# Performance work log

Hardware: AMD Instinct MI355X
Metric: run time of the kernel (lower is better)

## Reference

```python
import jax, jax.numpy as jnp
import numpy as np

SCALE = 1.0 / np.sqrt(1024.0).astype(np.float32)


def setup_inputs() -> dict:
    key = jax.random.key(0)
    k1, k2, k3, k4, k5, k6 = jax.random.split(key, 6)
    B, Lq, Lk, D_in, D = 8, 2048, 2048, 1024, 256
    data1 = jax.random.normal(k1, (B, Lq, D_in), dtype=jnp.float32)
    data2 = jax.random.normal(k2, (B, Lk, D), dtype=jnp.float32)
    Wq = jax.random.normal(k3, (D_in, D), dtype=jnp.float32) * (1.0 / np.sqrt(D_in))
    bq = jax.random.normal(k4, (D,), dtype=jnp.float32) * 0.01
    Wk = jax.random.normal(k5, (D, D), dtype=jnp.float32) * (1.0 / np.sqrt(D))
    bk = jax.random.normal(k6, (D,), dtype=jnp.float32) * 0.01
    return {"data1": data1, "data2": data2, "Wq": Wq, "bq": bq, "Wk": Wk, "bk": bk}


def reference(data1, data2, Wq, bq, Wk, bk):
    # query: [B, Lq, D], key: [B, Lk, D]
    query = jnp.einsum('bli,id->bld', data1, Wq) + bq
    key = jnp.einsum('bli,id->bld', data2, Wk) + bk
    # scores: [B, Lq, Lk], scaled by sqrt(1024) as in the original
    scores = jnp.einsum('bqd,bkd->bqk', query, key) * SCALE
    attn = jax.nn.softmax(scores, axis=-1)
    # key reused as value; fused residual add with query
    context = jnp.einsum('bqk,bkd->bqd', attn, key) + query
    return context
```

## Files before the change

kernel.cpp:

```cpp
#include <hip/hip_runtime.h>
#include <hip/hip_bf16.h>

typedef __bf16 bf16x8 __attribute__((ext_vector_type(8)));
typedef __bf16 bf16x2 __attribute__((ext_vector_type(2)));
typedef unsigned short u16x8 __attribute__((ext_vector_type(8)));
typedef float f32x4 __attribute__((ext_vector_type(4)));
typedef float f32x16 __attribute__((ext_vector_type(16)));

#define MFMA(a, b, c) __builtin_amdgcn_mfma_f32_16x16x32_bf16(a, b, c, 0, 0, 0)
#define MFMA32(a, b, c) __builtin_amdgcn_mfma_f32_32x32x16_bf16(a, b, c, 0, 0, 0)

#define LQ 2048
#define DD 256

static __device__ __forceinline__ float bf2f(unsigned short u) {
  union { unsigned int i; float f; } x; x.i = ((unsigned int)u) << 16; return x.f;
}
static __device__ __forceinline__ unsigned short f2bf(float f) {
  union { float f; unsigned int i; } x; x.f = f;
  unsigned int r = x.i + 0x7fffu + ((x.i >> 16) & 1u);
  return (unsigned short)(r >> 16);
}
static __device__ __forceinline__ void gll16(const void* g, void* l) {
  __builtin_amdgcn_global_load_lds(
      (const __attribute__((address_space(1))) unsigned int*)g,
      (__attribute__((address_space(3))) unsigned int*)l, 16, 0, 0);
}
static __device__ __forceinline__ unsigned pack2(float a, float b) {
  union { bf16x2 v; unsigned u; } x;
  x.v[0] = (__bf16)a; x.v[1] = (__bf16)b;
  return x.u;
}

__global__ void wt2_kernel(const float* __restrict__ Wq, unsigned short* __restrict__ WqT,
                           const float* __restrict__ Wk, unsigned short* __restrict__ WkT) {
  int id = blockIdx.x * 256 + threadIdx.x;
  if (id < 262144) {
    int n = id >> 10, k = id & 1023;
    WqT[id] = f2bf(Wq[k * 256 + n]);
  } else {
    int j = id - 262144;
    int n = j >> 8, k = j & 255;
    WkT[j] = f2bf(Wk[k * 256 + n]);
  }
}

static __device__ __forceinline__ void proj_body(
    const float* __restrict__ A, const unsigned short* __restrict__ WT,
    const float* __restrict__ bias, unsigned short* __restrict__ outb,
    unsigned short* __restrict__ outT, int Kd, int bid,
    unsigned short* A_s , unsigned short* B_s ) {
  const int tid = threadIdx.x;
  const int w = tid >> 6, lane = tid & 63, g = lane >> 4, c = lane & 15;
  const int m0 = (bid >> 1) * 64, n0 = (bid & 1) * 128;
  const int wr = (w >> 1) * 32, wc = (w & 1) * 64;

  f32x4 acc[2][4];
  const f32x4 z4 = {0.f, 0.f, 0.f, 0.f};
#pragma unroll
  for (int i = 0; i < 2; i++)
#pragma unroll
    for (int j = 0; j < 4; j++) acc[i][j] = z4;

  const int row_a = tid >> 2, k0a = (tid & 3) * 8;
  const unsigned swz_a = (unsigned)((row_a & 7) << 4);
  const float* asrc = A + (long)(m0 + row_a) * Kd + k0a;
  const int brow0 = w * 32 + (lane >> 2);

#define GLLB(buf, ks_)                                                         \
  _Pragma("unroll") for (int j = 0; j < 2; j++) {                              \
    const int brow = brow0 + j * 16;                                           \
    gll16((const char*)WT + (long)(n0 + brow) * (long)(Kd * 2) + (ks_) * 64 +  \
              (((lane & 3) * 16) ^ ((brow & 3) << 4)),                         \
          (char*)B_s + (buf) * 8192 + w * 2048 + j * 1024);                    \
  }

#define WRA(buf, plo, phi)                                                     \
  {                                                                            \
    bf16x8 t;                                                                  \
    _Pragma("unroll") for (int jj = 0; jj < 4; jj++) {                         \
      t[jj] = (__bf16)(plo)[jj]; t[4 + jj] = (__bf16)(phi)[jj];                \
    }                                                                          \
    *(bf16x8*)((char*)A_s + (buf) * 4096 +                                     \
               (((unsigned)(row_a * 64 + k0a * 2)) ^ swz_a)) = t;              \
  }

#define COMPUTE(buf)                                                           \
  {                                                                            \
    bf16x8 af[2], bfr[4];                                                      \
    _Pragma("unroll") for (int rf = 0; rf < 2; rf++) {                         \
      const int row = wr + rf * 16 + c;                                        \
      af[rf] = *(const bf16x8*)((char*)A_s + (buf) * 4096 +                    \
               (((unsigned)(row * 64 + g * 16)) ^ ((row & 7) << 4)));          \
    }                                                                          \
    _Pragma("unroll") for (int cf = 0; cf < 4; cf++) {                         \
      const int row = wc + cf * 16 + c;                                        \
      bfr[cf] = *(const bf16x8*)((char*)B_s + (buf) * 8192 + row * 64 +        \
               (((unsigned)(g * 16)) ^ ((unsigned)((row & 3) << 4))));         \
    }                                                                          \
    _Pragma("unroll") for (int rf = 0; rf < 2; rf++)                           \
      _Pragma("unroll") for (int cf = 0; cf < 4; cf++)                         \
        acc[rf][cf] = MFMA(af[rf], bfr[cf], acc[rf][cf]);                      \
  }

  const int nk = Kd >> 5;
  f32x4 pe0, pe1, po0, po1;
  pe0 = *(const f32x4*)(asrc);       pe1 = *(const f32x4*)(asrc + 4);
  GLLB(0, 0);
  po0 = *(const f32x4*)(asrc + 32);  po1 = *(const f32x4*)(asrc + 36);
  WRA(0, pe0, pe1);
  pe0 = *(const f32x4*)(asrc + 64);  pe1 = *(const f32x4*)(asrc + 68);
  __syncthreads();

  for (int t = 0; t < nk; t += 2) {
    GLLB(1, t + 1);
    WRA(1, po0, po1);
    if (t + 3 < nk) {
      po0 = *(const f32x4*)(asrc + (t + 3) * 32);
      po1 = *(const f32x4*)(asrc + (t + 3) * 32 + 4);
    }
    COMPUTE(0);
    __syncthreads();
    if (t + 2 < nk) {
      GLLB(0, t + 2);
      WRA(0, pe0, pe1);
      if (t + 4 < nk) {
        pe0 = *(const f32x4*)(asrc + (t + 4) * 32);
        pe1 = *(const f32x4*)(asrc + (t + 4) * 32 + 4);
      }
    }
    COMPUTE(1);
    __syncthreads();
  }
#undef GLLB
#undef WRA
#undef COMPUTE

#pragma unroll
  for (int cf = 0; cf < 4; cf++) {
    const int col = n0 + wc + cf * 16 + c;
    const float bv = bias[col];
#pragma unroll
    for (int rf = 0; rf < 2; rf++) {
      const int row0 = m0 + wr + rf * 16 + g * 4;
      unsigned short pk[4];
#pragma unroll
      for (int i = 0; i < 4; i++) {
        float v = acc[rf][cf][i] + bv;
        pk[i] = f2bf(v);
        outb[(long)(row0 + i) * 256 + col] = pk[i];
      }
      if (outT) {
        const int b = row0 >> 11;
        const int key0 = row0 & 2047;
        unsigned long long packed = (unsigned long long)pk[0] |
                                    ((unsigned long long)pk[1] << 16) |
                                    ((unsigned long long)pk[2] << 32) |
                                    ((unsigned long long)pk[3] << 48);
        *(unsigned long long*)(outT + ((long)(b * 256 + col) * LQ + key0)) = packed;
      }
    }
  }
}

__global__ __launch_bounds__(256) void proj2_kernel(
    const float* __restrict__ data1, const unsigned short* __restrict__ WqT,
    const float* __restrict__ bq, unsigned short* __restrict__ Qb,
    const float* __restrict__ data2, const unsigned short* __restrict__ WkT,
    const float* __restrict__ bk, unsigned short* __restrict__ Kb,
    unsigned short* __restrict__ KTb) {
  __shared__ unsigned short A_s[2 * 64 * 32];
  __shared__ unsigned short B_s[2 * 128 * 32];
  const int bid = blockIdx.x;
  if (bid < 512) {
    proj_body(data1, WqT, bq, Qb, (unsigned short*)nullptr, 1024, bid, A_s, B_s);
  } else {
    proj_body(data2, WkT, bk, Kb, KTb, 256, bid - 512, A_s, B_s);
  }
}

template <int NSPLIT, bool ALLBF>
__global__ __launch_bounds__(256, 2) void attn_kernel(
    const unsigned short* __restrict__ Qb, const unsigned short* __restrict__ Kb,
    const unsigned short* __restrict__ KTb, unsigned short* __restrict__ Op,
    float* __restrict__ out, float* __restrict__ ML) {
  constexpr int KS = 2048 / NSPLIT;
  constexpr int NT = KS / 32;
  constexpr int NBLK = 128 * NSPLIT;
  __shared__ char Ks[2][16384];
  __shared__ char KTs[2][16384];
  const int tid = threadIdx.x;
  const int w = tid >> 6, lane = tid & 63;
  const int l5 = lane >> 5, q31 = lane & 31;
  const int lid = (blockIdx.x & 7) * (NBLK / 8) + (blockIdx.x >> 3);
  const int ksplit = lid & (NSPLIT - 1), qg = lid / NSPLIT;
  const int b = qg >> 4;
  const long qrow0 = (long)qg * 128;
  const int kbase = ksplit * KS;
  const float CS = 0.03125f * 1.4426950408889634f;
  const float THRM = 8.0f / CS;

  bf16x8 qf[16];
  {
    const unsigned short* qp = Qb + (qrow0 + w * 32 + q31) * DD + l5 * 8;
#pragma unroll
    for (int s = 0; s < 16; s++) qf[s] = *(const bf16x8*)(qp + s * 16);
  }
  f32x16 o[8];
#pragma unroll
  for (int t = 0; t < 8; t++) o[t] = (f32x16)(0.f);
  float m_ = -1e30f, l_ = 0.f;

  const char* kb_b = (const char*)(Kb + (long)b * LQ * DD);
  const char* kt_b = (const char*)(KTb + (long)b * DD * LQ);

#define STAGE(buf, kt_)                                                          \
  {                                                                              \
    const int k0_ = kbase + (kt_) * 32;                                          \
    const char* kbp_ = kb_b + (long)(k0_ + q31) * 512 + l5 * 16;                 \
    _Pragma("unroll") for (int i = 0; i < 4; i++) {                              \
      const int sl = w * 4 + i;                                                  \
      gll16(kbp_ + sl * 32, Ks[buf] + sl * 1024);                                \
    }                                                                            \
    _Pragma("unroll") for (int i = 0; i < 4; i++) {                              \
      const int th = w * 4 + i;                                                  \
      gll16(kt_b + (long)((th >> 1) * 32 + q31) * 4096 + (long)k0_ * 2 +         \
                (th & 1) * 32 + l5 * 16,                                         \
            KTs[buf] + th * 1024);                                               \
    }                                                                            \
  }

  STAGE(0, 0);
  for (int kt = 0; kt < NT; kt++) {
    const int cur = kt & 1;
    __syncthreads();
    if (kt + 1 < NT) STAGE(cur ^ 1, kt + 1);

    const char* kr = Ks[cur] + lane * 16;
    f32x16 s = (f32x16)(0.f);
#pragma unroll
    for (int sl = 0; sl < 16; sl++) {
      bf16x8 kf = *(const bf16x8*)(kr + sl * 1024);
      s = MFMA32(kf, qf[sl], s);
    }

    float mx = s[0];
#pragma unroll
    for (int r = 1; r < 16; r++) mx = fmaxf(mx, s[r]);
    mx = fmaxf(mx, __shfl_xor(mx, 32));
    if (__any(mx > m_ + THRM)) {
      float mn = fmaxf(m_, mx);
      float al = exp2f((m_ - mn) * CS);
      m_ = mn;
      l_ *= al;
#pragma unroll
      for (int t = 0; t < 8; t++) o[t] *= al;
    }
    const float mCS = m_ * CS;
    float p[16];
    float ls = 0.f;
#pragma unroll
    for (int r = 0; r < 16; r++) {
      p[r] = exp2f(s[r] * CS - mCS);
      ls += p[r];
    }
    l_ += ls;

    unsigned pk[8];
#pragma unroll
    for (int j = 0; j < 8; j++) pk[j] = pack2(p[2 * j], p[2 * j + 1]);
    unsigned x0 = (unsigned)__shfl_xor((int)pk[0], 32);
    unsigned x1 = (unsigned)__shfl_xor((int)pk[1], 32);
    unsigned x2 = (unsigned)__shfl_xor((int)pk[2], 32);
    unsigned x3 = (unsigned)__shfl_xor((int)pk[3], 32);
    unsigned x4 = (unsigned)__shfl_xor((int)pk[4], 32);
    unsigned x5 = (unsigned)__shfl_xor((int)pk[5], 32);
    unsigned x6 = (unsigned)__shfl_xor((int)pk[6], 32);
    unsigned x7 = (unsigned)__shfl_xor((int)pk[7], 32);
    union { unsigned u[4]; bf16x8 v; } pf0, pf1;
    const bool hi = (l5 != 0);
    pf0.u[0] = hi ? x2 : pk[0];
    pf0.u[1] = hi ? x3 : pk[1];
    pf0.u[2] = hi ? pk[2] : x0;
    pf0.u[3] = hi ? pk[3] : x1;
    pf1.u[0] = hi ? x6 : pk[4];
    pf1.u[1] = hi ? x7 : pk[5];
    pf1.u[2] = hi ? pk[6] : x4;
    pf1.u[3] = hi ? pk[7] : x5;

    const char* vr = KTs[cur] + lane * 16;
#pragma unroll
    for (int t = 0; t < 8; t++) {
      bf16x8 v0 = *(const bf16x8*)(vr + (t * 2) * 1024);
      bf16x8 v1 = *(const bf16x8*)(vr + (t * 2 + 1) * 1024);
      o[t] = MFMA32(v0, pf0.v, o[t]);
      o[t] = MFMA32(v1, pf1.v, o[t]);
    }
  }
#undef STAGE

  l_ += __shfl_xor(l_, 32);

  const long orow = (qrow0 + w * 32 + q31) * (long)DD;
  if (!ALLBF && ksplit == NSPLIT - 1) {
    float* op = out + orow;
#pragma unroll
    for (int t = 0; t < 8; t++)
#pragma unroll
      for (int r = 0; r < 16; r++)
        op[t * 32 + (r & 3) + 8 * (r >> 2) + 4 * l5] = o[t][r];
  } else {
    unsigned short* opb = Op + (long)ksplit * (16384 * 256) + orow;
#pragma unroll
    for (int t = 0; t < 8; t++)
#pragma unroll
      for (int r = 0; r < 16; r++)
        opb[t * 32 + (r & 3) + 8 * (r >> 2) + 4 * l5] = f2bf(o[t][r]);
  }
  if (lane < 32) {
    float* mlp = ML + (long)(qg * NSPLIT + ksplit) * 256;
    mlp[w * 32 + q31] = m_;
    mlp[128 + w * 32 + q31] = l_;
  }
}

template <int NSPLIT, bool ALLBF>
__global__ __launch_bounds__(256) void merge_kernel(
    const unsigned short* __restrict__ Op, const float* __restrict__ ML,
    const unsigned short* __restrict__ Qb, float* __restrict__ out) {
  const float CS = 0.03125f * 1.4426950408889634f;
  const long gid = (long)blockIdx.x * 256 + threadIdx.x;
  const long idx = gid * 8;
  const int row = (int)(idx >> 8);
  const int qg = row >> 7, qr = row & 127;
  const float* mlb = ML + (long)(qg * NSPLIT) * 256;
  float mv[NSPLIT], lv[NSPLIT];
#pragma unroll
  for (int k = 0; k < NSPLIT; k++) {
    mv[k] = mlb[k * 256 + qr];
    lv[k] = mlb[k * 256 + 128 + qr];
  }
  float M = mv[0];
#pragma unroll
  for (int k = 1; k < NSPLIT; k++) M = fmaxf(M, mv[k]);
  float ek[NSPLIT], wsum = 0.f;
#pragma unroll
  for (int k = 0; k < NSPLIT; k++) {
    ek[k] = exp2f((mv[k] - M) * CS);
    wsum += ek[k] * lv[k];
  }
  const float inv = 1.0f / wsum;
  float acc[8];
  if (ALLBF) {
#pragma unroll
    for (int e = 0; e < 8; e++) acc[e] = 0.f;
#pragma unroll
    for (int k = 0; k < NSPLIT; k++) {
      u16x8 p = *(const u16x8*)(Op + (long)k * (16384 * 256) + idx);
#pragma unroll
      for (int e = 0; e < 8; e++) acc[e] += ek[k] * bf2f(p[e]);
    }
  } else {
    f32x4 pa = *(const f32x4*)(out + idx);
    f32x4 pb = *(const f32x4*)(out + idx + 4);
#pragma unroll
    for (int e = 0; e < 4; e++) {
      acc[e] = ek[NSPLIT - 1] * pa[e];
      acc[4 + e] = ek[NSPLIT - 1] * pb[e];
    }
#pragma unroll
    for (int k = 0; k < NSPLIT - 1; k++) {
      u16x8 p = *(const u16x8*)(Op + (long)k * (16384 * 256) + idx);
#pragma unroll
      for (int e = 0; e < 8; e++) acc[e] += ek[k] * bf2f(p[e]);
    }
  }
  u16x8 qv = *(const u16x8*)(Qb + idx);
  f32x4 ra, rb;
#pragma unroll
  for (int e = 0; e < 4; e++) ra[e] = acc[e] * inv + bf2f(qv[e]);
#pragma unroll
  for (int e = 0; e < 4; e++) rb[e] = acc[4 + e] * inv + bf2f(qv[4 + e]);
  *(f32x4*)(out + idx) = ra;
  *(f32x4*)(out + idx + 4) = rb;
}

extern "C" void kernel_launch(void* const* d_in, const int* in_sizes, int n_in,
                              void* d_out, int out_size, void* d_ws, size_t ws_size,
                              hipStream_t stream) {
  (void)in_sizes; (void)n_in; (void)out_size;
  const float* data1 = (const float*)d_in[0];
  const float* data2 = (const float*)d_in[1];
  const float* Wq = (const float*)d_in[2];
  const float* bq = (const float*)d_in[3];
  const float* Wk = (const float*)d_in[4];
  const float* bk = (const float*)d_in[5];
  float* out = (float*)d_out;

  char* ws = (char*)d_ws;
  unsigned short* Qb  = (unsigned short*)(ws);
  unsigned short* Kb  = (unsigned short*)(ws + (8ull << 20));
  unsigned short* KTb = (unsigned short*)(ws + (16ull << 20));
  unsigned short* WqT = (unsigned short*)(ws + (24ull << 20));
  unsigned short* WkT = (unsigned short*)(ws + (24ull << 20) + (512u << 10));
  unsigned short* Op  = (unsigned short*)(ws + (25ull << 20));

  wt2_kernel<<<dim3(1280), dim3(256), 0, stream>>>(Wq, WqT, Wk, WkT);
  proj2_kernel<<<dim3(1024), dim3(256), 0, stream>>>(data1, WqT, bq, Qb,
                                                     data2, WkT, bk, Kb, KTb);

  if (ws_size >= (58ull << 20)) {
    float* MLb = (float*)(ws + (57ull << 20));
    attn_kernel<4, true><<<dim3(512), dim3(256), 0, stream>>>(Qb, Kb, KTb, Op, out, MLb);
    merge_kernel<4, true><<<dim3(2048), dim3(256), 0, stream>>>(Op, MLb, Qb, out);
  } else if (ws_size >= (50ull << 20)) {
    float* MLb = (float*)(ws + (49ull << 20));
    attn_kernel<4, false><<<dim3(512), dim3(256), 0, stream>>>(Qb, Kb, KTb, Op, out, MLb);
    merge_kernel<4, false><<<dim3(2048), dim3(256), 0, stream>>>(Op, MLb, Qb, out);
  } else {
    float* MLb = (float*)(ws + (33ull << 20));
    attn_kernel<2, false><<<dim3(256), dim3(256), 0, stream>>>(Qb, Kb, KTb, Op, out, MLb);
    merge_kernel<2, false><<<dim3(2048), dim3(256), 0, stream>>>(Op, MLb, Qb, out);
  }
}
```

Before: 103.3 us.

## Fuse split-K merge into attention kernel via last-arriving-block atomic counter

```diff
diff --git a/kernel.cpp b/kernel.cpp
--- a/kernel.cpp
+++ b/kernel.cpp
@@ -12,6 +12,7 @@
 
 #define LQ 2048
 #define DD 256
+#define OPSTRIDE (16384L * 256L)
 
 static __device__ __forceinline__ float bf2f(unsigned short u) {
   union { unsigned int i; float f; } x; x.i = ((unsigned int)u) << 16; return x.f;
@@ -179,16 +180,18 @@
   }
 }
 
-template <int NSPLIT, bool ALLBF>
+template <int NSPLIT, bool ALLBF, bool FUSEMERGE>
 __global__ __launch_bounds__(256, 2) void attn_kernel(
     const unsigned short* __restrict__ Qb, const unsigned short* __restrict__ Kb,
     const unsigned short* __restrict__ KTb, unsigned short* __restrict__ Op,
-    float* __restrict__ out, float* __restrict__ ML) {
+    float* __restrict__ out, float* __restrict__ ML,
+    unsigned int* __restrict__ cnt) {
   constexpr int KS = 2048 / NSPLIT;
   constexpr int NT = KS / 32;
   constexpr int NBLK = 128 * NSPLIT;
   __shared__ char Ks[2][16384];
   __shared__ char KTs[2][16384];
+  __shared__ unsigned mold_s;
   const int tid = threadIdx.x;
   const int w = tid >> 6, lane = tid & 63;
   const int l5 = lane >> 5, q31 = lane & 31;
@@ -302,7 +305,7 @@
   l_ += __shfl_xor(l_, 32);
 
   const long orow = (qrow0 + w * 32 + q31) * (long)DD;
-  if (!ALLBF && ksplit == NSPLIT - 1) {
+  if (!ALLBF && !FUSEMERGE && ksplit == NSPLIT - 1) {
     float* op = out + orow;
 #pragma unroll
     for (int t = 0; t < 8; t++)
@@ -310,7 +313,7 @@
       for (int r = 0; r < 16; r++)
         op[t * 32 + (r & 3) + 8 * (r >> 2) + 4 * l5] = o[t][r];
   } else {
-    unsigned short* opb = Op + (long)ksplit * (16384 * 256) + orow;
+    unsigned short* opb = Op + (long)ksplit * OPSTRIDE + orow;
 #pragma unroll
     for (int t = 0; t < 8; t++)
 #pragma unroll
@@ -321,6 +324,56 @@
     float* mlp = ML + (long)(qg * NSPLIT + ksplit) * 256;
     mlp[w * 32 + q31] = m_;
     mlp[128 + w * 32 + q31] = l_;
+  }
+
+  if (FUSEMERGE) {
+    __threadfence();
+    __syncthreads();
+    if (tid == 0) mold_s = atomicAdd(&cnt[qg], 1u);
+    __syncthreads();
+    if (mold_s == (unsigned)(NSPLIT - 1)) {
+      __threadfence();
+      const float* mlb = ML + (long)(qg * NSPLIT) * 256;
+#pragma unroll 4
+      for (int j = 0; j < 16; j++) {
+        const int ci = tid + j * 256;
+        const int qr = ci >> 5;
+        const long idx = qrow0 * 256 + (long)ci * 8;
+        float mv[NSPLIT], lv[NSPLIT];
+#pragma unroll
+        for (int k = 0; k < NSPLIT; k++) {
+          mv[k] = mlb[k * 256 + qr];
+          lv[k] = mlb[k * 256 + 128 + qr];
+        }
+        float M = mv[0];
+#pragma unroll
+        for (int k = 1; k < NSPLIT; k++) M = fmaxf(M, mv[k]);
+        float ek[NSPLIT], wsum = 0.f;
+#pragma unroll
+        for (int k = 0; k < NSPLIT; k++) {
+          ek[k] = exp2f((mv[k] - M) * CS);
+          wsum += ek[k] * lv[k];
+        }
+        const float inv = 1.0f / wsum;
+        float acc[8];
+#pragma unroll
+        for (int e = 0; e < 8; e++) acc[e] = 0.f;
+#pragma unroll
+        for (int k = 0; k < NSPLIT; k++) {
+          u16x8 p = *(const u16x8*)(Op + (long)k * OPSTRIDE + idx);
+#pragma unroll
+          for (int e = 0; e < 8; e++) acc[e] += ek[k] * bf2f(p[e]);
+        }
+        u16x8 qv = *(const u16x8*)(Qb + idx);
+        f32x4 ra, rb;
+#pragma unroll
+        for (int e = 0; e < 4; e++) ra[e] = acc[e] * inv + bf2f(qv[e]);
+#pragma unroll
+        for (int e = 0; e < 4; e++) rb[e] = acc[4 + e] * inv + bf2f(qv[4 + e]);
+        *(f32x4*)(out + idx) = ra;
+        *(f32x4*)(out + idx + 4) = rb;
+      }
+    }
   }
 }
 
@@ -356,7 +409,7 @@
     for (int e = 0; e < 8; e++) acc[e] = 0.f;
 #pragma unroll
     for (int k = 0; k < NSPLIT; k++) {
-      u16x8 p = *(const u16x8*)(Op + (long)k * (16384 * 256) + idx);
+      u16x8 p = *(const u16x8*)(Op + (long)k * OPSTRIDE + idx);
 #pragma unroll
       for (int e = 0; e < 8; e++) acc[e] += ek[k] * bf2f(p[e]);
     }
@@ -370,7 +423,7 @@
     }
 #pragma unroll
     for (int k = 0; k < NSPLIT - 1; k++) {
-      u16x8 p = *(const u16x8*)(Op + (long)k * (16384 * 256) + idx);
+      u16x8 p = *(const u16x8*)(Op + (long)k * OPSTRIDE + idx);
 #pragma unroll
       for (int e = 0; e < 8; e++) acc[e] += ek[k] * bf2f(p[e]);
     }
@@ -411,15 +464,19 @@
 
   if (ws_size >= (58ull << 20)) {
     float* MLb = (float*)(ws + (57ull << 20));
-    attn_kernel<4, true><<<dim3(512), dim3(256), 0, stream>>>(Qb, Kb, KTb, Op, out, MLb);
-    merge_kernel<4, true><<<dim3(2048), dim3(256), 0, stream>>>(Op, MLb, Qb, out);
+    unsigned int* cnt = (unsigned int*)(ws + (57ull << 20) + (512u << 10));
+    hipMemsetAsync(cnt, 0, 128 * sizeof(unsigned int), stream);
+    attn_kernel<4, true, true><<<dim3(512), dim3(256), 0, stream>>>(
+        Qb, Kb, KTb, Op, out, MLb, cnt);
   } else if (ws_size >= (50ull << 20)) {
     float* MLb = (float*)(ws + (49ull << 20));
-    attn_kernel<4, false><<<dim3(512), dim3(256), 0, stream>>>(Qb, Kb, KTb, Op, out, MLb);
+    attn_kernel<4, false, false><<<dim3(512), dim3(256), 0, stream>>>(
+        Qb, Kb, KTb, Op, out, MLb, (unsigned int*)nullptr);
     merge_kernel<4, false><<<dim3(2048), dim3(256), 0, stream>>>(Op, MLb, Qb, out);
   } else {
     float* MLb = (float*)(ws + (33ull << 20));
-    attn_kernel<2, false><<<dim3(256), dim3(256), 0, stream>>>(Qb, Kb, KTb, Op, out, MLb);
+    attn_kernel<2, false, false><<<dim3(256), dim3(256), 0, stream>>>(
+        Qb, Kb, KTb, Op, out, MLb, (unsigned int*)nullptr);
     merge_kernel<2, false><<<dim3(2048), dim3(256), 0, stream>>>(Op, MLb, Qb, out);
   }
 }
```

Measured after the change: 197.0 us. +90.7%, slower.
